# Performance work log

Measured on AMD Instinct MI355X. Metric: run time of the kernel, lower is better.

The kernel has to match this reference:

```python
import jax, jax.numpy as jnp
import numpy as np

B, L, C, H = 8, 1024, 384, 6
D = C // H          # head_dim = 64
K, N = 2, 4         # radial_degree, angular_degree
EPS = 1e-5


def setup_inputs() -> dict:
    key = jax.random.key(0)
    ks = jax.random.split(key, 8)
    x = jax.random.normal(ks[0], (B, L, C), dtype=jnp.float32)
    pos = jax.random.uniform(ks[1], (B, L, 2), dtype=jnp.float32) * 32.0
    w_norm = jnp.ones((C,), dtype=jnp.float32)
    w_in = jax.random.normal(ks[2], (3 * C, C), dtype=jnp.float32) * 0.02
    b_in = jnp.zeros((3 * C,), dtype=jnp.float32)
    w_out = jax.random.normal(ks[3], (C, C), dtype=jnp.float32) * 0.02
    b_out = jnp.zeros((C,), dtype=jnp.float32)
    b_coef = jax.random.normal(ks[4], (H, K + 1, N + 1), dtype=jnp.float32) * 0.01
    b_coef = b_coef.at[:, 1, 0].set(1.0)  # reset_parameters fills b[..., 1, 0] = 1
    c_coef = jax.random.normal(ks[5], (H, K + 1, N + 1), dtype=jnp.float32) * 0.01
    return {"x": x, "pos": pos, "w_norm": w_norm, "w_in": w_in, "b_in": b_in,
            "w_out": w_out, "b_out": b_out, "b_coef": b_coef, "c_coef": c_coef}


def _polar_bias(pos, b_coef, c_coef):
    # pos: (B, L, 2) -> bias grid (B, H, L, L)
    dist = pos[:, :, None, :] - pos[:, None, :, :]           # (B, Lq, Lk, 2)
    theta = jnp.arctan2(dist[..., 1], dist[..., 0])          # (B, Lq, Lk)
    r = jnp.sqrt(jnp.sum(dist * dist, axis=-1))              # (B, Lq, Lk)
    r_pow = r[..., None] ** jnp.arange(K + 1, dtype=r.dtype)           # (B, Lq, Lk, K+1)
    ang = theta[..., None] * jnp.arange(N + 1, dtype=theta.dtype)      # (B, Lq, Lk, N+1)
    cos_part = jnp.einsum('hkn,bijk,bijn->bhij', b_coef, r_pow, jnp.cos(ang))
    sin_part = jnp.einsum('hkn,bijk,bijn->bhij', c_coef, r_pow, jnp.sin(ang))
    return cos_part + sin_part


def reference(x, pos, w_norm, w_in, b_in, w_out, b_out, b_coef, c_coef):
    # RMSNorm
    ms = jnp.mean(x * x, axis=-1, keepdims=True)
    xn = x * jax.lax.rsqrt(ms + EPS) * w_norm
    # packed QKV projection
    qkv = xn @ w_in.T + b_in                                  # (B, L, 3C)
    q, k, v = jnp.split(qkv, 3, axis=-1)
    def heads(t):  # (B, L, C) -> (B, H, L, D)
        return t.reshape(B, L, H, D).transpose(0, 2, 1, 3)
    q, k, v = heads(q), heads(k), heads(v)
    bias = _polar_bias(pos, b_coef, c_coef)                   # (B, H, L, L)
    scores = jnp.einsum('bhqd,bhkd->bhqk', q, k) / jnp.sqrt(jnp.float32(D)) + bias
    attn = jax.nn.softmax(scores, axis=-1)
    o = jnp.einsum('bhqk,bhkd->bhqd', attn, v)                # (B, H, L, D)
    o = o.transpose(0, 2, 1, 3).reshape(B, L, C)
    return o @ w_out.T + b_out
```

## Files before the change

### kernel.cpp

```cpp
#include <hip/hip_runtime.h>

typedef unsigned int  u32;
typedef unsigned short u16;
typedef __attribute__((ext_vector_type(8))) short short8;
typedef __attribute__((ext_vector_type(4))) float f32x4;

__device__ __forceinline__ u16 f2bf(float x) {
  union { float f; u32 u; } un; un.f = x;
  u32 r = un.u + 0x7FFFu + ((un.u >> 16) & 1u);
  return (u16)(r >> 16);
}
__device__ __forceinline__ u32 cvtpk(float lo, float hi) {
  u32 r;
  asm("v_cvt_pk_bf16_f32 %0, %1, %2" : "=v"(r) : "v"(lo), "v"(hi));
  return r;
}
__device__ __forceinline__ f32x4 mfma_bf16(short8 a, short8 b, f32x4 c) {
  return __builtin_amdgcn_mfma_f32_16x16x32_bf16(a, b, c, 0, 0, 0);
}

__global__ __launch_bounds__(256) void prep_kernel(
    const float* __restrict__ x, const float* __restrict__ w_norm,
    const float* __restrict__ w_in, const float* __restrict__ w_out,
    u16* __restrict__ xn, u16* __restrict__ winb, u16* __restrict__ woutb)
{
  int blk = blockIdx.x, t = threadIdx.x;
  if (blk < 2048) {
    int wv = t >> 6, lane = t & 63;
    int row = blk * 4 + wv;
    const float* xr = x + (size_t)row * 384;
    float v[6]; float ss = 0.f;
    #pragma unroll
    for (int i = 0; i < 6; i++) { v[i] = xr[lane + 64 * i]; ss += v[i] * v[i]; }
    #pragma unroll
    for (int off = 32; off > 0; off >>= 1) ss += __shfl_xor(ss, off);
    float rs = __builtin_amdgcn_rsqf(ss * (1.0f / 384.0f) + 1e-5f);
    #pragma unroll
    for (int i = 0; i < 6; i++) {
      float xv = v[i] * rs * w_norm[lane + 64 * i];
      xn[(size_t)row * 384 + lane + 64 * i] = f2bf(xv);
    }
  } else {
    int base = (blk - 2048) * 2048 + t * 8;
    #pragma unroll
    for (int j = 0; j < 8; j++) {
      int idx = base + j;
      if (idx < 442368) winb[idx] = f2bf(w_in[idx]);
      else              woutb[idx - 442368] = f2bf(w_out[idx - 442368]);
    }
  }
}

template<bool OUT_F32, bool QSCALE>
__global__ __launch_bounds__(256) void gemm_kernel(
    const u16* __restrict__ A, int lda,
    const u16* __restrict__ Bw, int ldb,
    const float* __restrict__ bias, void* __restrict__ outp, int ldc, int K)
{
  __shared__ __attribute__((aligned(16))) u16 As[128 * 72];
  __shared__ __attribute__((aligned(16))) u16 Bs[128 * 72];
  int t = threadIdx.x;
  int lane = t & 63, wv = t >> 6;
  int g = lane >> 4, cl = lane & 15;
  int row0 = blockIdx.x * 128, col0 = blockIdx.y * 128;
  int wm = (wv >> 1) * 64, wn = (wv & 1) * 64;
  f32x4 acc[4][4];
  #pragma unroll
  for (int i = 0; i < 4; i++)
    #pragma unroll
    for (int j = 0; j < 4; j++) acc[i][j] = (f32x4){0.f, 0.f, 0.f, 0.f};

  for (int k0 = 0; k0 < K; k0 += 64) {
    __syncthreads();
    #pragma unroll
    for (int j = 0; j < 4; j++) {
      int i = t + 256 * j;
      int r = i >> 3, ch = i & 7;
      *(uint4*)(&As[r * 72 + ch * 8]) =
          *(const uint4*)(A + (size_t)(row0 + r) * lda + k0 + ch * 8);
      *(uint4*)(&Bs[r * 72 + ch * 8]) =
          *(const uint4*)(Bw + (size_t)(col0 + r) * ldb + k0 + ch * 8);
    }
    __syncthreads();
    #pragma unroll
    for (int kh = 0; kh < 2; kh++) {
      short8 af[4], bfr[4];
      #pragma unroll
      for (int s = 0; s < 4; s++) {
        af[s]  = *(const short8*)(&As[(wm + s * 16 + cl) * 72 + kh * 32 + g * 8]);
        bfr[s] = *(const short8*)(&Bs[(wn + s * 16 + cl) * 72 + kh * 32 + g * 8]);
      }
      #pragma unroll
      for (int i = 0; i < 4; i++)
        #pragma unroll
        for (int j = 0; j < 4; j++)
          acc[i][j] = mfma_bf16(af[i], bfr[j], acc[i][j]);
    }
  }
  #pragma unroll
  for (int i = 0; i < 4; i++) {
    #pragma unroll
    for (int j = 0; j < 4; j++) {
      int colb = col0 + wn + j * 16 + cl;
      float bv = bias[colb];
      #pragma unroll
      for (int r = 0; r < 4; r++) {
        int rowb = row0 + wm + i * 16 + g * 4 + r;
        float v = acc[i][j][r] + bv;
        if (QSCALE) { if (colb < 384) v *= 0.125f; }
        if (OUT_F32) ((float*)outp)[(size_t)rowb * ldc + colb] = v;
        else ((u16*)outp)[(size_t)rowb * ldc + colb] = f2bf(v);
      }
    }
  }
}

__global__ __launch_bounds__(256) void attn_swap4(
    const u16* __restrict__ qkv, const float* __restrict__ pos,
    const float* __restrict__ bcf, const float* __restrict__ ccf,
    u16* __restrict__ obuf)
{
  __shared__ __attribute__((aligned(16))) u16 vsmem[4][64][40];

  int bid = blockIdx.x;
  int xslot = bid & 7, rest = bid >> 3;
  int qt16 = rest & 63, gdiv = rest >> 6;
  int g48 = gdiv * 8 + xslot;
  int b = g48 / 6, h = g48 - b * 6;

  int t = threadIdx.x, lane = t & 63, wv = t >> 6;
  int g = lane >> 4, cl = lane & 15;

  float bc[15], cc[15];
  #pragma unroll
  for (int i = 0; i < 15; i++) { bc[i] = bcf[h * 15 + i]; cc[i] = ccf[h * 15 + i]; }

  int qrow = qt16 * 16 + cl;
  const u16* qbase = qkv + (size_t)(b * 1024 + qrow) * 1152 + h * 64;
  short8 qf0 = *(const short8*)(qbase + g * 8);
  short8 qf1 = *(const short8*)(qbase + 32 + g * 8);
  float qx = pos[(size_t)(b * 1024 + qrow) * 2 + 0];
  float qy = pos[(size_t)(b * 1024 + qrow) * 2 + 1];

  f32x4 oa[4];
  #pragma unroll
  for (int d = 0; d < 4; d++) oa[d] = (f32x4){0.f, 0.f, 0.f, 0.f};
  float m_own = -1e30f, l_own = 0.f;

  const u16* kb = qkv + (size_t)b * 1024 * 1152 + 384 + h * 64;
  int kappa = lane & 31, dh = lane >> 5;
  const u16* vb = qkv + (size_t)b * 1024 * 1152 + 768 + h * 64 + dh * 32;
  const float* pb = pos + (size_t)b * 2048;

  int pcol = (kappa & 3) | ((kappa & 0x0C) << 1) | ((kappa & 0x10) >> 2);
  u16* vdst = &vsmem[wv][dh * 32][0] + pcol;

  u32 koff = (u32)(wv * 256 + cl) * 1152;
  u32 voff = (u32)(wv * 256 + kappa) * 1152;
  u32 poff = (u32)(wv * 256 + 4 * g) * 2;

  for (int it = 0; it < 8; it++) {
    {
      const u16* vr = vb + voff;
      uint4 a0 = *(const uint4*)(vr);
      uint4 a1 = *(const uint4*)(vr + 8);
      uint4 a2 = *(const uint4*)(vr + 16);
      uint4 a3 = *(const uint4*)(vr + 24);
      #define ST(i, val) vdst[(i) * 40] = (u16)(val)
      ST(0,  a0.x); ST(1,  a0.x >> 16); ST(2,  a0.y); ST(3,  a0.y >> 16);
      ST(4,  a0.z); ST(5,  a0.z >> 16); ST(6,  a0.w); ST(7,  a0.w >> 16);
      ST(8,  a1.x); ST(9,  a1.x >> 16); ST(10, a1.y); ST(11, a1.y >> 16);
      ST(12, a1.z); ST(13, a1.z >> 16); ST(14, a1.w); ST(15, a1.w >> 16);
      ST(16, a2.x); ST(17, a2.x >> 16); ST(18, a2.y); ST(19, a2.y >> 16);
      ST(20, a2.z); ST(21, a2.z >> 16); ST(22, a2.w); ST(23, a2.w >> 16);
      ST(24, a3.x); ST(25, a3.x >> 16); ST(26, a3.y); ST(27, a3.y >> 16);
      ST(28, a3.z); ST(29, a3.z >> 16); ST(30, a3.w); ST(31, a3.w >> 16);
      #undef ST
    }
    f32x4 sk[2];
    #pragma unroll
    for (int ks = 0; ks < 2; ks++) {
      const u16* kr = kb + koff + ks * (16 * 1152);
      short8 kf0 = *(const short8*)(kr + g * 8);
      short8 kf1 = *(const short8*)(kr + 32 + g * 8);
      f32x4 z = (f32x4){0.f, 0.f, 0.f, 0.f};
      z = mfma_bf16(kf0, qf0, z);
      z = mfma_bf16(kf1, qf1, z);
      sk[ks] = z;
    }
    #pragma unroll
    for (int ks = 0; ks < 2; ks++) {
      float4 pA = *(const float4*)(pb + poff + ks * 32);
      float4 pB = *(const float4*)(pb + poff + ks * 32 + 4);
      float kxs[4] = {pA.x, pA.z, pB.x, pB.z};
      float kys[4] = {pA.y, pA.w, pB.y, pB.w};
      #pragma unroll
      for (int r = 0; r < 4; r++) {
        float dx = qx - kxs[r], dy = qy - kys[r];
        float r2 = dx * dx + dy * dy;
        bool zz = !(r2 > 0.f);
        float ir = zz ? 0.f : __builtin_amdgcn_rsqf(r2);
        float rr = r2 * ir;
        float c1 = zz ? 1.f : dx * ir;
        float s1 = dy * ir;
        float tc = c1 + c1;
        float c2 = __builtin_fmaf(tc, c1, -1.f), s2 = tc * s1;
        float c3 = __builtin_fmaf(tc, c2, -c1),  s3 = __builtin_fmaf(tc, s2, -s1);
        float c4 = __builtin_fmaf(tc, c3, -c2),  s4 = __builtin_fmaf(tc, s3, -s2);
        float a0 = bc[0] + bc[1]*c1 + bc[2]*c2 + bc[3]*c3 + bc[4]*c4
                 + cc[1]*s1 + cc[2]*s2 + cc[3]*s3 + cc[4]*s4;
        float a1 = bc[5] + bc[6]*c1 + bc[7]*c2 + bc[8]*c3 + bc[9]*c4
                 + cc[6]*s1 + cc[7]*s2 + cc[8]*s3 + cc[9]*s4;
        float a2 = bc[10] + bc[11]*c1 + bc[12]*c2 + bc[13]*c3 + bc[14]*c4
                 + cc[11]*s1 + cc[12]*s2 + cc[13]*s3 + cc[14]*s4;
        sk[ks][r] += a0 + rr * __builtin_fmaf(rr, a2, a1);
      }
    }
    koff += 32 * 1152; voff += 32 * 1152; poff += 64;
    float tmax = -1e30f;
    #pragma unroll
    for (int ks = 0; ks < 2; ks++)
      #pragma unroll
      for (int r = 0; r < 4; r++) tmax = fmaxf(tmax, sk[ks][r]);
    if (!__all((int)(tmax <= m_own + 8.f))) {
      tmax = fmaxf(tmax, __shfl_xor(tmax, 16));
      tmax = fmaxf(tmax, __shfl_xor(tmax, 32));
      float mn = fmaxf(m_own, tmax);
      float sc = __builtin_amdgcn_exp2f((m_own - mn) * 1.44269504f);
      m_own = mn;
      l_own *= sc;
      #pragma unroll
      for (int r = 0; r < 4; r++) {
        float scr = __shfl(sc, 4 * g + r);
        #pragma unroll
        for (int d = 0; d < 4; d++) oa[d][r] *= scr;
      }
    }
    float psum = 0.f;
    #pragma unroll
    for (int ks = 0; ks < 2; ks++)
      #pragma unroll
      for (int r = 0; r < 4; r++) {
        float p = __builtin_amdgcn_exp2f((sk[ks][r] - m_own) * 1.44269504f);
        psum += p; sk[ks][r] = p;
      }
    l_own += psum;
    union { u32 w[4]; short8 s8; } pk;
    pk.w[0] = cvtpk(sk[0][0], sk[0][1]); pk.w[1] = cvtpk(sk[0][2], sk[0][3]);
    pk.w[2] = cvtpk(sk[1][0], sk[1][1]); pk.w[3] = cvtpk(sk[1][2], sk[1][3]);
    #pragma unroll
    for (int d = 0; d < 4; d++) {
      short8 vf = *(const short8*)(&vsmem[wv][d * 16 + cl][g * 8]);
      oa[d] = mfma_bf16(pk.s8, vf, oa[d]);
    }
  }
  l_own += __shfl_xor(l_own, 16);
  l_own += __shfl_xor(l_own, 32);
  __syncthreads();
  float* o1 = (float*)&vsmem[0][0][0];
  float* ml = (float*)((char*)&vsmem[0][0][0] + 19968);
  if (lane < 16) { ml[wv * 16 + lane] = m_own; ml[64 + wv * 16 + lane] = l_own; }
  if (wv > 0) {
    #pragma unroll
    for (int r = 0; r < 4; r++) {
      int row = 4 * g + r;
      #pragma unroll
      for (int d = 0; d < 4; d++)
        o1[((wv - 1) * 16 + row) * 64 + d * 16 + cl] = oa[d][r];
    }
  }
  __syncthreads();
  if (wv == 0) {
    float m1 = ml[16 + cl], m2 = ml[32 + cl], m3 = ml[48 + cl];
    float l1 = ml[80 + cl], l2 = ml[96 + cl], l3 = ml[112 + cl];
    float M  = fmaxf(fmaxf(m_own, m1), fmaxf(m2, m3));
    float f0 = __builtin_amdgcn_exp2f((m_own - M) * 1.44269504f);
    float f1 = __builtin_amdgcn_exp2f((m1 - M) * 1.44269504f);
    float f2 = __builtin_amdgcn_exp2f((m2 - M) * 1.44269504f);
    float f3 = __builtin_amdgcn_exp2f((m3 - M) * 1.44269504f);
    float linv = __builtin_amdgcn_rcpf(l_own * f0 + l1 * f1 + l2 * f2 + l3 * f3);
    #pragma unroll
    for (int r = 0; r < 4; r++) {
      int row = 4 * g + r;
      float f0r = __shfl(f0, row), f1r = __shfl(f1, row);
      float f2r = __shfl(f2, row), f3r = __shfl(f3, row);
      float invr = __shfl(linv, row);
      int qr = qt16 * 16 + row;
      #pragma unroll
      for (int d = 0; d < 4; d++) {
        float val = (oa[d][r] * f0r
                   + o1[(0 * 16 + row) * 64 + d * 16 + cl] * f1r
                   + o1[(1 * 16 + row) * 64 + d * 16 + cl] * f2r
                   + o1[(2 * 16 + row) * 64 + d * 16 + cl] * f3r) * invr;
        obuf[(size_t)(b * 1024 + qr) * 384 + h * 64 + d * 16 + cl] = f2bf(val);
      }
    }
  }
}

extern "C" void kernel_launch(void* const* d_in, const int* in_sizes, int n_in,
                              void* d_out, int out_size, void* d_ws, size_t ws_size,
                              hipStream_t stream) {
  const float* x      = (const float*)d_in[0];
  const float* pos    = (const float*)d_in[1];
  const float* w_norm = (const float*)d_in[2];
  const float* w_in   = (const float*)d_in[3];
  const float* b_in   = (const float*)d_in[4];
  const float* w_out  = (const float*)d_in[5];
  const float* b_out  = (const float*)d_in[6];
  const float* b_coef = (const float*)d_in[7];
  const float* c_coef = (const float*)d_in[8];

  char* ws = (char*)d_ws;
  u16* xn    = (u16*)(ws + 0);
  u16* obuf  = (u16*)(ws + 0);
  u16* winb  = (u16*)(ws + 6291456);
  u16* woutb = (u16*)(ws + 7176192);
  u16* qkvb  = (u16*)(ws + 7471104);

  prep_kernel<<<2336, 256, 0, stream>>>(x, w_norm, w_in, w_out, xn, winb, woutb);
  gemm_kernel<false, true><<<dim3(64, 9), 256, 0, stream>>>(
      xn, 384, winb, 384, b_in, qkvb, 1152, 384);
  attn_swap4<<<3072, 256, 0, stream>>>(qkvb, pos, b_coef, c_coef, obuf);
  gemm_kernel<true, false><<<dim3(64, 3), 256, 0, stream>>>(
      obuf, 384, woutb, 384, b_out, (float*)d_out, 384, 384);
}
```

Baseline: 156.4 us.

## Prefetch next K/V/pos tiles into registers and pack bias math as float2

The attention loop now loads the next iteration's K fragments, V rows and key positions into registers while the current tile is being computed. The next V tile is staged into the per-wave LDS buffer after the P·V MFMAs instead of at the top of the loop, so global load latency can overlap with MFMA and bias arithmetic. The polar-bias evaluation for the two 16-key subtiles is rewritten with float2 vectors so the compiler can emit packed FP32 FMAs. The loop is fully unrolled. The extra live registers from double-buffering could lower occupancy.

```diff
diff --git a/kernel.cpp b/kernel.cpp
--- a/kernel.cpp
+++ b/kernel.cpp
@@ -4,6 +4,7 @@
 typedef unsigned short u16;
 typedef __attribute__((ext_vector_type(8))) short short8;
 typedef __attribute__((ext_vector_type(4))) float f32x4;
+typedef __attribute__((ext_vector_type(2))) float f32x2;
 
 __device__ __forceinline__ u16 f2bf(float x) {
   union { float f; u32 u; } un; un.f = x;
@@ -115,7 +116,7 @@
   }
 }
 
-__global__ __launch_bounds__(256) void attn_swap4(
+__global__ __launch_bounds__(256) void attn_swap5(
     const u16* __restrict__ qkv, const float* __restrict__ pos,
     const float* __restrict__ bcf, const float* __restrict__ ccf,
     u16* __restrict__ obuf)
@@ -159,64 +160,93 @@
   u32 voff = (u32)(wv * 256 + kappa) * 1152;
   u32 poff = (u32)(wv * 256 + 4 * g) * 2;
 
+  #define LOADV(d0,d1,d2,d3, off) { const u16* vr = vb + (off); \
+      d0 = *(const uint4*)(vr); d1 = *(const uint4*)(vr + 8); \
+      d2 = *(const uint4*)(vr + 16); d3 = *(const uint4*)(vr + 24); }
+  #define LOADK(ka0,ka1,kb0,kb1, off) { \
+      const u16* kr0 = kb + (off); const u16* kr1 = kr0 + 16 * 1152; \
+      ka0 = *(const short8*)(kr0 + g * 8); ka1 = *(const short8*)(kr0 + 32 + g * 8); \
+      kb0 = *(const short8*)(kr1 + g * 8); kb1 = *(const short8*)(kr1 + 32 + g * 8); }
+  #define LOADP(pa0,pb0,pa1,pb1, off) { \
+      pa0 = *(const float4*)(pb + (off));      pb0 = *(const float4*)(pb + (off) + 4); \
+      pa1 = *(const float4*)(pb + (off) + 32); pb1 = *(const float4*)(pb + (off) + 36); }
+  #define STAGE(d0,d1,d2,d3) { \
+      vdst[ 0*40]=(u16)(d0.x); vdst[ 1*40]=(u16)(d0.x>>16); \
+      vdst[ 2*40]=(u16)(d0.y); vdst[ 3*40]=(u16)(d0.y>>16); \
+      vdst[ 4*40]=(u16)(d0.z); vdst[ 5*40]=(u16)(d0.z>>16); \
+      vdst[ 6*40]=(u16)(d0.w); vdst[ 7*40]=(u16)(d0.w>>16); \
+      vdst[ 8*40]=(u16)(d1.x); vdst[ 9*40]=(u16)(d1.x>>16); \
+      vdst[10*40]=(u16)(d1.y); vdst[11*40]=(u16)(d1.y>>16); \
+      vdst[12*40]=(u16)(d1.z); vdst[13*40]=(u16)(d1.z>>16); \
+      vdst[14*40]=(u16)(d1.w); vdst[15*40]=(u16)(d1.w>>16); \
+      vdst[16*40]=(u16)(d2.x); vdst[17*40]=(u16)(d2.x>>16); \
+      vdst[18*40]=(u16)(d2.y); vdst[19*40]=(u16)(d2.y>>16); \
+      vdst[20*40]=(u16)(d2.z); vdst[21*40]=(u16)(d2.z>>16); \
+      vdst[22*40]=(u16)(d2.w); vdst[23*40]=(u16)(d2.w>>16); \
+      vdst[24*40]=(u16)(d3.x); vdst[25*40]=(u16)(d3.x>>16); \
+      vdst[26*40]=(u16)(d3.y); vdst[27*40]=(u16)(d3.y>>16); \
+      vdst[28*40]=(u16)(d3.z); vdst[29*40]=(u16)(d3.z>>16); \
+      vdst[30*40]=(u16)(d3.w); vdst[31*40]=(u16)(d3.w>>16); }
+
+  uint4 cv0, cv1, cv2, cv3; short8 ck00, ck01, ck10, ck11;
+  float4 cp00, cp01, cp10, cp11;
+  LOADV(cv0, cv1, cv2, cv3, voff);
+  LOADK(ck00, ck01, ck10, ck11, koff);
+  LOADP(cp00, cp01, cp10, cp11, poff);
+  STAGE(cv0, cv1, cv2, cv3);
+  voff += 32 * 1152; koff += 32 * 1152; poff += 64;
+
+  #pragma unroll
   for (int it = 0; it < 8; it++) {
+    uint4 nv0, nv1, nv2, nv3; short8 nk00, nk01, nk10, nk11;
+    float4 np00, np01, np10, np11;
+    if (it < 7) {
+      LOADV(nv0, nv1, nv2, nv3, voff);
+      LOADK(nk00, nk01, nk10, nk11, koff);
+      LOADP(np00, np01, np10, np11, poff);
+      voff += 32 * 1152; koff += 32 * 1152; poff += 64;
+    }
+    f32x4 sk[2];
     {
-      const u16* vr = vb + voff;
-      uint4 a0 = *(const uint4*)(vr);
-      uint4 a1 = *(const uint4*)(vr + 8);
-      uint4 a2 = *(const uint4*)(vr + 16);
-      uint4 a3 = *(const uint4*)(vr + 24);
-      #define ST(i, val) vdst[(i) * 40] = (u16)(val)
-      ST(0,  a0.x); ST(1,  a0.x >> 16); ST(2,  a0.y); ST(3,  a0.y >> 16);
-      ST(4,  a0.z); ST(5,  a0.z >> 16); ST(6,  a0.w); ST(7,  a0.w >> 16);
-      ST(8,  a1.x); ST(9,  a1.x >> 16); ST(10, a1.y); ST(11, a1.y >> 16);
-      ST(12, a1.z); ST(13, a1.z >> 16); ST(14, a1.w); ST(15, a1.w >> 16);
-      ST(16, a2.x); ST(17, a2.x >> 16); ST(18, a2.y); ST(19, a2.y >> 16);
-      ST(20, a2.z); ST(21, a2.z >> 16); ST(22, a2.w); ST(23, a2.w >> 16);
-      ST(24, a3.x); ST(25, a3.x >> 16); ST(26, a3.y); ST(27, a3.y >> 16);
-      ST(28, a3.z); ST(29, a3.z >> 16); ST(30, a3.w); ST(31, a3.w >> 16);
-      #undef ST
-    }
-    f32x4 sk[2];
-    #pragma unroll
-    for (int ks = 0; ks < 2; ks++) {
-      const u16* kr = kb + koff + ks * (16 * 1152);
-      short8 kf0 = *(const short8*)(kr + g * 8);
-      short8 kf1 = *(const short8*)(kr + 32 + g * 8);
       f32x4 z = (f32x4){0.f, 0.f, 0.f, 0.f};
-      z = mfma_bf16(kf0, qf0, z);
-      z = mfma_bf16(kf1, qf1, z);
-      sk[ks] = z;
-    }
-    #pragma unroll
-    for (int ks = 0; ks < 2; ks++) {
-      float4 pA = *(const float4*)(pb + poff + ks * 32);
-      float4 pB = *(const float4*)(pb + poff + ks * 32 + 4);
-      float kxs[4] = {pA.x, pA.z, pB.x, pB.z};
-      float kys[4] = {pA.y, pA.w, pB.y, pB.w};
+      z = mfma_bf16(ck00, qf0, z); z = mfma_bf16(ck01, qf1, z);
+      sk[0] = z;
+      z = (f32x4){0.f, 0.f, 0.f, 0.f};
+      z = mfma_bf16(ck10, qf0, z); z = mfma_bf16(ck11, qf1, z);
+      sk[1] = z;
+    }
+    {
+      float kx0[4] = {cp00.x, cp00.z, cp01.x, cp01.z};
+      float ky0[4] = {cp00.y, cp00.w, cp01.y, cp01.w};
+      float kx1[4] = {cp10.x, cp10.z, cp11.x, cp11.z};
+      float ky1[4] = {cp10.y, cp10.w, cp11.y, cp11.w};
       #pragma unroll
       for (int r = 0; r < 4; r++) {
-        float dx = qx - kxs[r], dy = qy - kys[r];
-        float r2 = dx * dx + dy * dy;
-        bool zz = !(r2 > 0.f);
-        float ir = zz ? 0.f : __builtin_amdgcn_rsqf(r2);
-        float rr = r2 * ir;
-        float c1 = zz ? 1.f : dx * ir;
-        float s1 = dy * ir;
-        float tc = c1 + c1;
-        float c2 = __builtin_fmaf(tc, c1, -1.f), s2 = tc * s1;
-        float c3 = __builtin_fmaf(tc, c2, -c1),  s3 = __builtin_fmaf(tc, s2, -s1);
-        float c4 = __builtin_fmaf(tc, c3, -c2),  s4 = __builtin_fmaf(tc, s3, -s2);
-        float a0 = bc[0] + bc[1]*c1 + bc[2]*c2 + bc[3]*c3 + bc[4]*c4
+        f32x2 dx = {qx - kx0[r], qx - kx1[r]};
+        f32x2 dy = {qy - ky0[r], qy - ky1[r]};
+        f32x2 r2 = dx * dx + dy * dy;
+        float ir0 = (r2.x > 0.f) ? __builtin_amdgcn_rsqf(r2.x) : 0.f;
+        float ir1 = (r2.y > 0.f) ? __builtin_amdgcn_rsqf(r2.y) : 0.f;
+        f32x2 ir = {ir0, ir1};
+        f32x2 rr = r2 * ir;
+        f32x2 c1 = {(r2.x > 0.f) ? dx.x * ir0 : 1.f,
+                    (r2.y > 0.f) ? dx.y * ir1 : 1.f};
+        f32x2 s1 = dy * ir;
+        f32x2 tc = c1 + c1;
+        f32x2 c2 = tc * c1 - 1.f, s2 = tc * s1;
+        f32x2 c3 = tc * c2 - c1,  s3 = tc * s2 - s1;
+        f32x2 c4 = tc * c3 - c2,  s4 = tc * s3 - s2;
+        f32x2 a0 = bc[0] + bc[1]*c1 + bc[2]*c2 + bc[3]*c3 + bc[4]*c4
                  + cc[1]*s1 + cc[2]*s2 + cc[3]*s3 + cc[4]*s4;
-        float a1 = bc[5] + bc[6]*c1 + bc[7]*c2 + bc[8]*c3 + bc[9]*c4
+        f32x2 a1 = bc[5] + bc[6]*c1 + bc[7]*c2 + bc[8]*c3 + bc[9]*c4
                  + cc[6]*s1 + cc[7]*s2 + cc[8]*s3 + cc[9]*s4;
-        float a2 = bc[10] + bc[11]*c1 + bc[12]*c2 + bc[13]*c3 + bc[14]*c4
+        f32x2 a2 = bc[10] + bc[11]*c1 + bc[12]*c2 + bc[13]*c3 + bc[14]*c4
                  + cc[11]*s1 + cc[12]*s2 + cc[13]*s3 + cc[14]*s4;
-        sk[ks][r] += a0 + rr * __builtin_fmaf(rr, a2, a1);
-      }
-    }
-    koff += 32 * 1152; voff += 32 * 1152; poff += 64;
+        f32x2 sv = a0 + rr * (a1 + rr * a2);
+        sk[0][r] += sv.x;
+        sk[1][r] += sv.y;
+      }
+    }
     float tmax = -1e30f;
     #pragma unroll
     for (int ks = 0; ks < 2; ks++)
@@ -253,7 +283,16 @@
       short8 vf = *(const short8*)(&vsmem[wv][d * 16 + cl][g * 8]);
       oa[d] = mfma_bf16(pk.s8, vf, oa[d]);
     }
-  }
+    if (it < 7) {
+      STAGE(nv0, nv1, nv2, nv3);
+      ck00 = nk00; ck01 = nk01; ck10 = nk10; ck11 = nk11;
+      cp00 = np00; cp01 = np01; cp10 = np10; cp11 = np11;
+    }
+  }
+  #undef LOADV
+  #undef LOADK
+  #undef LOADP
+  #undef STAGE
   l_own += __shfl_xor(l_own, 16);
   l_own += __shfl_xor(l_own, 32);
   __syncthreads();
@@ -321,7 +360,7 @@
   prep_kernel<<<2336, 256, 0, stream>>>(x, w_norm, w_in, w_out, xn, winb, woutb);
   gemm_kernel<false, true><<<dim3(64, 9), 256, 0, stream>>>(
       xn, 384, winb, 384, b_in, qkvb, 1152, 384);
-  attn_swap4<<<3072, 256, 0, stream>>>(qkvb, pos, b_coef, c_coef, obuf);
+  attn_swap5<<<3072, 256, 0, stream>>>(qkvb, pos, b_coef, c_coef, obuf);
   gemm_kernel<true, false><<<dim3(64, 3), 256, 0, stream>>>(
       obuf, 384, woutb, 384, b_out, (float*)d_out, 384, 384);
 }
```

Result: faster. 146.9 us, median of 2 (-6.1%).
